# Kernel tuning notes

Measured on AMD Instinct MI355X. Metric: run time of the kernel, lower is better.

The kernel has to match this reference:

```python
import jax, jax.numpy as jnp
import numpy as np

BLOCK = 64          # block_dim
GAPS = (1, 64)      # block_dim**i for i in range(num_layers=2), input_dim=4096
N_BLOCKS = 64       # input_dim // block_dim
HID = 128           # 2 * block_dim (hidden_layers_ratio=[2])
BS = 8192
IN_DIM = 4096


def setup_inputs() -> dict:
    key = jax.random.key(0)
    kx, kw1, kw2 = jax.random.split(key, 3)
    x = jax.random.normal(kx, (BS, IN_DIM), dtype=jnp.float32)
    # one BlockResMLP per factorized layer: BlockLinear(64, 64, 128) -> ELU -> BlockLinear(64, 128, 64)
    w1 = jax.random.normal(kw1, (len(GAPS), N_BLOCKS, BLOCK, HID), dtype=jnp.float32) / np.sqrt(BLOCK)
    b1 = jnp.zeros((len(GAPS), N_BLOCKS, 1, HID), dtype=jnp.float32)
    w2 = jax.random.normal(kw2, (len(GAPS), N_BLOCKS, HID, BLOCK), dtype=jnp.float32) / np.sqrt(HID)
    b2 = jnp.zeros((len(GAPS), N_BLOCKS, 1, BLOCK), dtype=jnp.float32)
    return {"x": x, "w1": w1, "b1": b1, "w2": w2, "b2": b2}


def _facto(y, w1, b1, w2, b2):
    # BlockResMLP.forward: view(bs, n_blocks, BLOCK).transpose(0,1) -> batched block GEMMs -> residual
    bs = y.shape[0]
    z = y.reshape(bs, -1, BLOCK).transpose(1, 0, 2)              # (n_blocks, bs, BLOCK)
    h = jnp.einsum('nbd,nde->nbe', z, w1) + b1                   # BlockLinear 1 + bias
    h = jax.nn.elu(h)                                            # ELU (alpha=1)
    h = jnp.einsum('nbe,ned->nbd', h, w2) + b2                   # BlockLinear 2 + bias
    z = h + z                                                    # residual
    return z.transpose(1, 0, 2).reshape(bs, -1)


def reference(x, w1, b1, w2, b2):
    bs = x.shape[0]
    y = x
    for i, gap in enumerate(GAPS):
        # permutation shuffle: view(-1, BLOCK, gap).transpose(2,1).contiguous().view(bs,-1)
        y = y.reshape(-1, BLOCK, gap).transpose(0, 2, 1).reshape(bs, -1)
        y = _facto(y, w1[i], b1[i], w2[i], b2[i])
        # inverse shuffle: view(-1, gap, BLOCK).transpose(2,1)
        y = y.reshape(-1, gap, BLOCK).transpose(0, 2, 1).reshape(bs, -1)
    return y
```

## Files before the change

### kernel.cpp

```cpp
#include <hip/hip_runtime.h>


typedef short short8 __attribute__((ext_vector_type(8)));
typedef short short4v __attribute__((ext_vector_type(4)));
typedef float floatx4 __attribute__((ext_vector_type(4)));
typedef unsigned int uintx4 __attribute__((ext_vector_type(4)));

#define MFMA(A, B, C) __builtin_amdgcn_mfma_f32_16x16x32_bf16((A), (B), (C), 0, 0, 0)

__device__ __forceinline__ unsigned short bf16r(float f) {
  unsigned int u = __builtin_bit_cast(unsigned int, f);
  u += 0x7FFFu + ((u >> 16) & 1u);
  return (unsigned short)(u >> 16);
}
__device__ __forceinline__ float bf16f(unsigned short h) {
  unsigned int u = ((unsigned int)h) << 16;
  return __builtin_bit_cast(float, u);
}
__device__ __forceinline__ unsigned int pk2(float lo, float hi) {
  return (unsigned int)bf16r(lo) | ((unsigned int)bf16r(hi) << 16);
}
__device__ __forceinline__ float eluf(float v) {
  return v > 0.f ? v : (__expf(v) - 1.f);
}
__device__ __forceinline__ uint4 gather44(const short* A, const short* B, int s) {
  uint4 o;
  o.x = (unsigned int)(unsigned short)A[0 * s] |
        ((unsigned int)(unsigned short)A[1 * s] << 16);
  o.y = (unsigned int)(unsigned short)A[2 * s] |
        ((unsigned int)(unsigned short)A[3 * s] << 16);
  o.z = (unsigned int)(unsigned short)B[0 * s] |
        ((unsigned int)(unsigned short)B[1 * s] << 16);
  o.w = (unsigned int)(unsigned short)B[2 * s] |
        ((unsigned int)(unsigned short)B[3 * s] << 16);
  return o;
}

__global__ __launch_bounds__(256) void k0_prep(const float* __restrict__ w1,
                                               const float* __restrict__ w2,
                                               short* __restrict__ w1t,
                                               short* __restrict__ w2t) {
  __shared__ __align__(16) short T[128 * 72];
  const int t  = threadIdx.x;
  const int ln = blockIdx.x >> 1;
  const bool pm = (ln >= 64);
  if ((blockIdx.x & 1) == 0) {
    const float* src = w1 + (size_t)ln * 8192 + t * 32;
    const int d = t >> 2, e0 = (t & 3) * 32;
#pragma unroll
    for (int u = 0; u < 32; u += 2) {
      *(unsigned int*)&T[d * 136 + e0 + u] = pk2(src[u], src[u + 1]);
    }
    __syncthreads();
    const int e = t >> 1, d0 = (t & 1) * 32;
    short* dst = w1t + (size_t)ln * 8192 + e * 64 + d0;
#pragma unroll
    for (int k = 0; k < 4; ++k) {
      const int ta = d0 + (pm ? 4 * k : 8 * k);
      const int tb = d0 + (pm ? 16 + 4 * k : 8 * k + 4);
      *(uint4*)(dst + k * 8) = gather44(&T[ta * 136 + e], &T[tb * 136 + e], 136);
    }
  } else {
    const float* src = w2 + (size_t)ln * 8192 + t * 32;
    const int e = t >> 1, d0 = (t & 1) * 32;
#pragma unroll
    for (int u = 0; u < 32; u += 2) {
      *(unsigned int*)&T[e * 72 + d0 + u] = pk2(src[u], src[u + 1]);
    }
    __syncthreads();
    const int dp = t >> 2, e0 = (t & 3) * 32;
    short* dst = w2t + (size_t)ln * 8192 + dp * 128 + e0;
#pragma unroll
    for (int k = 0; k < 4; ++k) {
      const int ta = e0 + (pm ? 4 * k : 8 * k);
      const int tb = e0 + (pm ? 16 + 4 * k : 8 * k + 4);
      *(uint4*)(dst + k * 8) = gather44(&T[ta * 72 + dp], &T[tb * 72 + dp], 72);
    }
  }
}

__global__ __launch_bounds__(256) void k1_layer0(
    const float* __restrict__ x,
    const short* __restrict__ w1t, const short* __restrict__ w2t,
    const float* __restrict__ b1,  const float* __restrict__ b2,
    short* __restrict__ y1) {
  __shared__ __align__(16) short hst[4][2][16][72];
  const int tid  = threadIdx.x;
  const int lane = tid & 63;
  const int wv   = tid >> 6;
  const int il   = lane & 15;
  const int q    = lane >> 4;
  const int npair   = blockIdx.x & 31;
  const int rowtile = blockIdx.x >> 5;
  const int n  = npair * 2 + (wv & 1);
  const int r0 = rowtile * 64 + (wv >> 1) * 32;

  const short* w1n = w1t + (size_t)n * 8192;
  const short* w2n = w2t + (size_t)n * 8192;
  const float* b1n = b1 + n * 128;
  const float* b2n = b2 + n * 64;

  short8 a[2][2];
#pragma unroll
  for (int Mt = 0; Mt < 2; ++Mt) {
#pragma unroll
    for (int ks = 0; ks < 2; ++ks) {
      const float* xp = x + (size_t)(r0 + Mt * 16 + il) * 4096 + n * 64 + ks * 32 + q * 8;
      floatx4 f0 = *(const floatx4*)xp;
      floatx4 f1 = *(const floatx4*)(xp + 4);
      short8 t;
#pragma unroll
      for (int u = 0; u < 4; ++u) { t[u] = (short)bf16r(f0[u]); t[4 + u] = (short)bf16r(f1[u]); }
      a[ks][Mt] = t;
    }
  }

  floatx4 acc2[2][4] = {};
  for (int hh = 0; hh < 2; ++hh) {
    floatx4 acc1[2][4] = {};
#pragma unroll
    for (int ks = 0; ks < 2; ++ks) {
#pragma unroll
      for (int nt = 0; nt < 4; ++nt) {
        short8 b = *(const short8*)(w1n + (hh * 64 + nt * 16 + il) * 64 + ks * 32 + q * 8);
        acc1[0][nt] = MFMA(a[ks][0], b, acc1[0][nt]);
        acc1[1][nt] = MFMA(a[ks][1], b, acc1[1][nt]);
      }
    }
#pragma unroll
    for (int nt = 0; nt < 4; ++nt) {
      float bias = b1n[hh * 64 + nt * 16 + il];
#pragma unroll
      for (int Mt = 0; Mt < 2; ++Mt)
#pragma unroll
        for (int rg = 0; rg < 4; ++rg) {
          float v = acc1[Mt][nt][rg] + bias;
          hst[wv][Mt][q * 4 + rg][nt * 16 + il] = (short)bf16r(eluf(v));
        }
    }
    asm volatile("s_waitcnt lgkmcnt(0)" ::: "memory");
#pragma unroll
    for (int ks2 = 0; ks2 < 2; ++ks2) {
      short8 a2[2];
      a2[0] = *(const short8*)&hst[wv][0][il][ks2 * 32 + q * 8];
      a2[1] = *(const short8*)&hst[wv][1][il][ks2 * 32 + q * 8];
#pragma unroll
      for (int nt2 = 0; nt2 < 4; ++nt2) {
        short8 b = *(const short8*)(w2n + (nt2 * 16 + il) * 128 + hh * 64 + ks2 * 32 + q * 8);
        acc2[0][nt2] = MFMA(a2[0], b, acc2[0][nt2]);
        acc2[1][nt2] = MFMA(a2[1], b, acc2[1][nt2]);
      }
    }
    asm volatile("s_waitcnt lgkmcnt(0)" ::: "memory");
  }
#pragma unroll
  for (int Mt = 0; Mt < 2; ++Mt) {
    const int R0 = r0 + Mt * 16 + q * 4;
    const size_t nbase = ((size_t)((r0 + Mt * 16) >> 4) * 64 + n) * 64;
#pragma unroll
    for (int nt2 = 0; nt2 < 4; ++nt2) {
      const int j = nt2 * 16 + il;
      const float bias = b2n[j];
      float v0 = acc2[Mt][nt2][0] + bias + x[(size_t)(R0 + 0) * 4096 + n * 64 + j];
      float v1 = acc2[Mt][nt2][1] + bias + x[(size_t)(R0 + 1) * 4096 + n * 64 + j];
      float v2 = acc2[Mt][nt2][2] + bias + x[(size_t)(R0 + 2) * 4096 + n * 64 + j];
      float v3 = acc2[Mt][nt2][3] + bias + x[(size_t)(R0 + 3) * 4096 + n * 64 + j];
      uint2 pk;
      pk.x = pk2(v0, v1);
      pk.y = pk2(v2, v3);
      *(uint2*)(y1 + (nbase + j) * 16 + q * 4) = pk;
    }
  }
}

#define RSTR 1156
#define ISTR 18
__global__ __launch_bounds__(256) void k2_layer1_out(
    const short* __restrict__ y1,
    const short* __restrict__ w1t, const short* __restrict__ w2t,
    const float* __restrict__ b1,  const float* __restrict__ b2,
    float* __restrict__ out) {
  __shared__ __align__(16) short yo[16 * RSTR];
  const int tid  = threadIdx.x;
  const int lane = tid & 63;
  const int wv   = tid >> 6;
  const int il   = lane & 15;
  const int q    = lane >> 4;
  const int G    = blockIdx.x & 511;
  const int m0   = (blockIdx.x >> 9) * 16;

  short8 pb;
#pragma unroll
  for (int v = 0; v < 8; ++v) pb[v] = (v < 4 && il == q * 4 + v) ? (short)0x3F80 : (short)0;
  const floatx4 zero4 = {0.f, 0.f, 0.f, 0.f};

#pragma unroll
  for (int mi = 0; mi < 4; ++mi) {
    const int ml = wv * 4 + mi;
    const int m  = m0 + ml;
    const short* w1m = w1t + (size_t)(64 + m) * 8192;
    const short* w2m = w2t + (size_t)(64 + m) * 8192;
    const float* b1m = b1 + (64 + m) * 128;
    const float* b2m = b2 + (64 + m) * 64;

    short4v za[4];
#pragma unroll
    for (int nt = 0; nt < 4; ++nt)
      za[nt] = *(const short4v*)(y1 + ((size_t)(G * 64 + nt * 16 + il) * 64 + m) * 16 + q * 4);

    floatx4 zd[4];
#pragma unroll
    for (int nt = 0; nt < 4; ++nt) {
      short8 az = {za[nt][0], za[nt][1], za[nt][2], za[nt][3], 0, 0, 0, 0};
      zd[nt] = MFMA(az, pb, zero4);
    }
    short8 at[2];
#pragma unroll
    for (int ks = 0; ks < 2; ++ks) {
      uintx4 w;
      w[0] = pk2(zd[2 * ks][0], zd[2 * ks][1]);
      w[1] = pk2(zd[2 * ks][2], zd[2 * ks][3]);
      w[2] = pk2(zd[2 * ks + 1][0], zd[2 * ks + 1][1]);
      w[3] = pk2(zd[2 * ks + 1][2], zd[2 * ks + 1][3]);
      at[ks] = __builtin_bit_cast(short8, w);
    }

    floatx4 acc2[4] = {};
    uintx4 a2w[4];
#pragma unroll
    for (int hh = 0; hh < 2; ++hh) {
      floatx4 acc1[4] = {};
#pragma unroll
      for (int ks = 0; ks < 2; ++ks)
#pragma unroll
        for (int nt = 0; nt < 4; ++nt) {
          short8 b = *(const short8*)(w1m + (hh * 64 + nt * 16 + il) * 64 + ks * 32 + q * 8);
          acc1[nt] = MFMA(at[ks], b, acc1[nt]);
        }
#pragma unroll
      for (int nt = 0; nt < 4; ++nt) {
        const float bias = b1m[hh * 64 + nt * 16 + il];
        short8 ha = {(short)bf16r(eluf(acc1[nt][0] + bias)),
                     (short)bf16r(eluf(acc1[nt][1] + bias)),
                     (short)bf16r(eluf(acc1[nt][2] + bias)),
                     (short)bf16r(eluf(acc1[nt][3] + bias)),
                     0, 0, 0, 0};
        floatx4 hd = MFMA(ha, pb, zero4);
        const int ks2 = hh * 2 + (nt >> 1);
        const int hf  = nt & 1;
        a2w[ks2][hf * 2 + 0] = pk2(hd[0], hd[1]);
        a2w[ks2][hf * 2 + 1] = pk2(hd[2], hd[3]);
      }
    }
#pragma unroll
    for (int ks2 = 0; ks2 < 4; ++ks2) {
      short8 af = __builtin_bit_cast(short8, a2w[ks2]);
#pragma unroll
      for (int nt2 = 0; nt2 < 4; ++nt2) {
        short8 b = *(const short8*)(w2m + (nt2 * 16 + il) * 128 + ks2 * 32 + q * 8);
        acc2[nt2] = MFMA(af, b, acc2[nt2]);
      }
    }
#pragma unroll
    for (int nt2 = 0; nt2 < 4; ++nt2) {
      const int i = nt2 * 16 + il;
      const float bias = b2m[i];
#pragma unroll
      for (int rg = 0; rg < 4; ++rg) {
        float val = acc2[nt2][rg] + bias + bf16f((unsigned short)za[nt2][rg]);
        yo[(q * 4 + rg) * RSTR + i * ISTR + ml] = (short)bf16r(val);
      }
    }
  }
  __syncthreads();

  const int r  = tid & 15;
  const int i0 = (tid >> 4) * 4;
  float* orow = out + (size_t)(G * 16 + r) * 4096 + m0;
#pragma unroll
  for (int k = 0; k < 4; ++k) {
    const int i = i0 + k;
    const short* yr = &yo[r * RSTR + i * ISTR];
    float f[16];
#pragma unroll
    for (int j = 0; j < 8; ++j) {
      unsigned int w = *(const unsigned int*)(yr + 2 * j);
      f[2 * j]     = bf16f((unsigned short)(w & 0xffffu));
      f[2 * j + 1] = bf16f((unsigned short)(w >> 16));
    }
    float* op = orow + i * 64;
    *(floatx4*)(op + 0)  = (floatx4){f[0],  f[1],  f[2],  f[3]};
    *(floatx4*)(op + 4)  = (floatx4){f[4],  f[5],  f[6],  f[7]};
    *(floatx4*)(op + 8)  = (floatx4){f[8],  f[9],  f[10], f[11]};
    *(floatx4*)(op + 12) = (floatx4){f[12], f[13], f[14], f[15]};
  }
}

extern "C" void kernel_launch(void* const* d_in, const int* in_sizes, int n_in,
                              void* d_out, int out_size, void* d_ws, size_t ws_size,
                              hipStream_t stream) {
  const float* x  = (const float*)d_in[0];
  const float* w1 = (const float*)d_in[1];
  const float* b1 = (const float*)d_in[2];
  const float* w2 = (const float*)d_in[3];
  const float* b2 = (const float*)d_in[4];
  float* out = (float*)d_out;

  short* w1t = (short*)d_ws;
  short* w2t = w1t + (1u << 20);
  short* y1  = w2t + (1u << 20);

  hipLaunchKernelGGL(k0_prep,       dim3(256),  dim3(256), 0, stream, w1, w2, w1t, w2t);
  hipLaunchKernelGGL(k1_layer0,     dim3(4096), dim3(256), 0, stream, x, w1t, w2t, b1, b2, y1);
  hipLaunchKernelGGL(k2_layer1_out, dim3(2048), dim3(256), 0, stream, y1, w1t, w2t, b1, b2, out);
}
```

Measured before the change: 466.7 us.

## Keep layer-0 hidden activations in registers and restructure layer-1 output blocks

Layer 0 now re-lays out the ELU hidden tile through a permutation MFMA instead of an LDS round trip, and rebuilds the residual from the already-loaded bf16 input fragments instead of re-reading fp32 x from global memory. The w2 prep always uses the permuted k-order to match the new A-fragment layout. Layer 1 moves to 1024-thread blocks where each wave owns one block index m across four row groups, with double-buffered LDS staging and a sync per group so output stores are 16-byte coalesced per row. The residual now uses bf16-rounded x, which changes numerics slightly, and the per-group barriers add synchronisation.

```diff
diff --git a/kernel.cpp b/kernel.cpp
--- a/kernel.cpp
+++ b/kernel.cpp
@@ -43,8 +43,8 @@
   __shared__ __align__(16) short T[128 * 72];
   const int t  = threadIdx.x;
   const int ln = blockIdx.x >> 1;
-  const bool pm = (ln >= 64);
   if ((blockIdx.x & 1) == 0) {
+    const bool pm = (ln >= 64);
     const float* src = w1 + (size_t)ln * 8192 + t * 32;
     const int d = t >> 2, e0 = (t & 3) * 32;
 #pragma unroll
@@ -72,8 +72,8 @@
     short* dst = w2t + (size_t)ln * 8192 + dp * 128 + e0;
 #pragma unroll
     for (int k = 0; k < 4; ++k) {
-      const int ta = e0 + (pm ? 4 * k : 8 * k);
-      const int tb = e0 + (pm ? 16 + 4 * k : 8 * k + 4);
+      const int ta = e0 + 4 * k;
+      const int tb = e0 + 16 + 4 * k;
       *(uint4*)(dst + k * 8) = gather44(&T[ta * 72 + dp], &T[tb * 72 + dp], 72);
     }
   }
@@ -84,7 +84,6 @@
     const short* __restrict__ w1t, const short* __restrict__ w2t,
     const float* __restrict__ b1,  const float* __restrict__ b2,
     short* __restrict__ y1) {
-  __shared__ __align__(16) short hst[4][2][16][72];
   const int tid  = threadIdx.x;
   const int lane = tid & 63;
   const int wv   = tid >> 6;
@@ -100,6 +99,11 @@
   const float* b1n = b1 + n * 128;
   const float* b2n = b2 + n * 64;
 
+  const floatx4 zero4 = {0.f, 0.f, 0.f, 0.f};
+  short8 pbH;
+#pragma unroll
+  for (int v = 0; v < 8; ++v) pbH[v] = (v < 4 && il == q * 4 + v) ? (short)0x3F80 : (short)0;
+
   short8 a[2][2];
 #pragma unroll
   for (int Mt = 0; Mt < 2; ++Mt) {
@@ -127,91 +131,113 @@
         acc1[1][nt] = MFMA(a[ks][1], b, acc1[1][nt]);
       }
     }
-#pragma unroll
-    for (int nt = 0; nt < 4; ++nt) {
-      float bias = b1n[hh * 64 + nt * 16 + il];
-#pragma unroll
-      for (int Mt = 0; Mt < 2; ++Mt)
-#pragma unroll
-        for (int rg = 0; rg < 4; ++rg) {
-          float v = acc1[Mt][nt][rg] + bias;
-          hst[wv][Mt][q * 4 + rg][nt * 16 + il] = (short)bf16r(eluf(v));
-        }
-    }
-    asm volatile("s_waitcnt lgkmcnt(0)" ::: "memory");
-#pragma unroll
-    for (int ks2 = 0; ks2 < 2; ++ks2) {
-      short8 a2[2];
-      a2[0] = *(const short8*)&hst[wv][0][il][ks2 * 32 + q * 8];
-      a2[1] = *(const short8*)&hst[wv][1][il][ks2 * 32 + q * 8];
+    uintx4 a2w[2][2];
+#pragma unroll
+    for (int Mt = 0; Mt < 2; ++Mt) {
+#pragma unroll
+      for (int nt = 0; nt < 4; ++nt) {
+        const float bias = b1n[hh * 64 + nt * 16 + il];
+        short8 ha = {(short)bf16r(eluf(acc1[Mt][nt][0] + bias)),
+                     (short)bf16r(eluf(acc1[Mt][nt][1] + bias)),
+                     (short)bf16r(eluf(acc1[Mt][nt][2] + bias)),
+                     (short)bf16r(eluf(acc1[Mt][nt][3] + bias)),
+                     0, 0, 0, 0};
+        floatx4 hd = MFMA(ha, pbH, zero4);
+        const int ks2l = nt >> 1;
+        const int hf   = nt & 1;
+        a2w[Mt][ks2l][hf * 2 + 0] = pk2(hd[0], hd[1]);
+        a2w[Mt][ks2l][hf * 2 + 1] = pk2(hd[2], hd[3]);
+      }
+    }
+#pragma unroll
+    for (int ks2l = 0; ks2l < 2; ++ks2l) {
+      short8 af0 = __builtin_bit_cast(short8, a2w[0][ks2l]);
+      short8 af1 = __builtin_bit_cast(short8, a2w[1][ks2l]);
 #pragma unroll
       for (int nt2 = 0; nt2 < 4; ++nt2) {
-        short8 b = *(const short8*)(w2n + (nt2 * 16 + il) * 128 + hh * 64 + ks2 * 32 + q * 8);
-        acc2[0][nt2] = MFMA(a2[0], b, acc2[0][nt2]);
-        acc2[1][nt2] = MFMA(a2[1], b, acc2[1][nt2]);
-      }
-    }
-    asm volatile("s_waitcnt lgkmcnt(0)" ::: "memory");
+        short8 b = *(const short8*)(w2n + (nt2 * 16 + il) * 128 + hh * 64 + ks2l * 32 + q * 8);
+        acc2[0][nt2] = MFMA(af0, b, acc2[0][nt2]);
+        acc2[1][nt2] = MFMA(af1, b, acc2[1][nt2]);
+      }
+    }
+  }
+
+  short8 pb0, pb1;
+#pragma unroll
+  for (int v = 0; v < 8; ++v) {
+    pb0[v] = (q * 8 + v == il)      ? (short)0x3F80 : (short)0;
+    pb1[v] = (q * 8 + v == il + 16) ? (short)0x3F80 : (short)0;
   }
 #pragma unroll
   for (int Mt = 0; Mt < 2; ++Mt) {
-    const int R0 = r0 + Mt * 16 + q * 4;
     const size_t nbase = ((size_t)((r0 + Mt * 16) >> 4) * 64 + n) * 64;
 #pragma unroll
-    for (int nt2 = 0; nt2 < 4; ++nt2) {
-      const int j = nt2 * 16 + il;
-      const float bias = b2n[j];
-      float v0 = acc2[Mt][nt2][0] + bias + x[(size_t)(R0 + 0) * 4096 + n * 64 + j];
-      float v1 = acc2[Mt][nt2][1] + bias + x[(size_t)(R0 + 1) * 4096 + n * 64 + j];
-      float v2 = acc2[Mt][nt2][2] + bias + x[(size_t)(R0 + 2) * 4096 + n * 64 + j];
-      float v3 = acc2[Mt][nt2][3] + bias + x[(size_t)(R0 + 3) * 4096 + n * 64 + j];
-      uint2 pk;
-      pk.x = pk2(v0, v1);
-      pk.y = pk2(v2, v3);
-      *(uint2*)(y1 + (nbase + j) * 16 + q * 4) = pk;
+    for (int ks = 0; ks < 2; ++ks) {
+      floatx4 xr[2];
+      xr[0] = MFMA(a[ks][Mt], pb0, zero4);
+      xr[1] = MFMA(a[ks][Mt], pb1, zero4);
+#pragma unroll
+      for (int h = 0; h < 2; ++h) {
+        const int nt2 = ks * 2 + h;
+        const int j = nt2 * 16 + il;
+        const float bias = b2n[j];
+        uint2 pk;
+        pk.x = pk2(acc2[Mt][nt2][0] + bias + xr[h][0],
+                   acc2[Mt][nt2][1] + bias + xr[h][1]);
+        pk.y = pk2(acc2[Mt][nt2][2] + bias + xr[h][2],
+                   acc2[Mt][nt2][3] + bias + xr[h][3]);
+        *(uint2*)(y1 + (nbase + j) * 16 + q * 4) = pk;
+      }
     }
   }
 }
 
 #define RSTR 1156
 #define ISTR 18
-__global__ __launch_bounds__(256) void k2_layer1_out(
+__global__ __launch_bounds__(1024) void k2_layer1_out(
     const short* __restrict__ y1,
     const short* __restrict__ w1t, const short* __restrict__ w2t,
     const float* __restrict__ b1,  const float* __restrict__ b2,
     float* __restrict__ out) {
-  __shared__ __align__(16) short yo[16 * RSTR];
+  __shared__ __align__(16) short yo[2][16 * RSTR];
   const int tid  = threadIdx.x;
   const int lane = tid & 63;
   const int wv   = tid >> 6;
   const int il   = lane & 15;
   const int q    = lane >> 4;
-  const int G    = blockIdx.x & 511;
-  const int m0   = (blockIdx.x >> 9) * 16;
+  const int rowband = blockIdx.x & 127;
+  const int m0      = (blockIdx.x >> 7) * 16;
+  const int m       = m0 + wv;
 
   short8 pb;
 #pragma unroll
   for (int v = 0; v < 8; ++v) pb[v] = (v < 4 && il == q * 4 + v) ? (short)0x3F80 : (short)0;
   const floatx4 zero4 = {0.f, 0.f, 0.f, 0.f};
 
-#pragma unroll
-  for (int mi = 0; mi < 4; ++mi) {
-    const int ml = wv * 4 + mi;
-    const int m  = m0 + ml;
-    const short* w1m = w1t + (size_t)(64 + m) * 8192;
-    const short* w2m = w2t + (size_t)(64 + m) * 8192;
-    const float* b1m = b1 + (64 + m) * 128;
-    const float* b2m = b2 + (64 + m) * 64;
-
-    short4v za[4];
+  const short* w1m = w1t + (size_t)(64 + m) * 8192;
+  const short* w2m = w2t + (size_t)(64 + m) * 8192;
+  const float* b1m = b1 + (64 + m) * 128;
+  const float* b2m = b2 + (64 + m) * 64;
+
+  short4v za[4][4];
+#pragma unroll
+  for (int g = 0; g < 4; ++g) {
+    const int G = rowband * 4 + g;
 #pragma unroll
     for (int nt = 0; nt < 4; ++nt)
-      za[nt] = *(const short4v*)(y1 + ((size_t)(G * 64 + nt * 16 + il) * 64 + m) * 16 + q * 4);
-
+      za[g][nt] = *(const short4v*)(y1 + ((size_t)(G * 64 + nt * 16 + il) * 64 + m) * 16 + q * 4);
+  }
+
+  const int fmq = tid & 3;
+  const int fiw = (tid >> 2) & 63;
+  const int frr = tid >> 8;
+
+#pragma unroll
+  for (int g = 0; g < 4; ++g) {
     floatx4 zd[4];
 #pragma unroll
     for (int nt = 0; nt < 4; ++nt) {
-      short8 az = {za[nt][0], za[nt][1], za[nt][2], za[nt][3], 0, 0, 0, 0};
+      short8 az = {za[g][nt][0], za[g][nt][1], za[g][nt][2], za[g][nt][3], 0, 0, 0, 0};
       zd[nt] = MFMA(az, pb, zero4);
     }
     short8 at[2];
@@ -261,38 +287,33 @@
         acc2[nt2] = MFMA(af, b, acc2[nt2]);
       }
     }
+    short* yob = &yo[g & 1][0];
 #pragma unroll
     for (int nt2 = 0; nt2 < 4; ++nt2) {
       const int i = nt2 * 16 + il;
       const float bias = b2m[i];
 #pragma unroll
       for (int rg = 0; rg < 4; ++rg) {
-        float val = acc2[nt2][rg] + bias + bf16f((unsigned short)za[nt2][rg]);
-        yo[(q * 4 + rg) * RSTR + i * ISTR + ml] = (short)bf16r(val);
-      }
-    }
-  }
-  __syncthreads();
-
-  const int r  = tid & 15;
-  const int i0 = (tid >> 4) * 4;
-  float* orow = out + (size_t)(G * 16 + r) * 4096 + m0;
-#pragma unroll
-  for (int k = 0; k < 4; ++k) {
-    const int i = i0 + k;
-    const short* yr = &yo[r * RSTR + i * ISTR];
-    float f[16];
-#pragma unroll
-    for (int j = 0; j < 8; ++j) {
-      unsigned int w = *(const unsigned int*)(yr + 2 * j);
-      f[2 * j]     = bf16f((unsigned short)(w & 0xffffu));
-      f[2 * j + 1] = bf16f((unsigned short)(w >> 16));
-    }
-    float* op = orow + i * 64;
-    *(floatx4*)(op + 0)  = (floatx4){f[0],  f[1],  f[2],  f[3]};
-    *(floatx4*)(op + 4)  = (floatx4){f[4],  f[5],  f[6],  f[7]};
-    *(floatx4*)(op + 8)  = (floatx4){f[8],  f[9],  f[10], f[11]};
-    *(floatx4*)(op + 12) = (floatx4){f[12], f[13], f[14], f[15]};
+        float val = acc2[nt2][rg] + bias + bf16f((unsigned short)za[g][nt2][rg]);
+        yob[(q * 4 + rg) * RSTR + i * ISTR + wv] = (short)bf16r(val);
+      }
+    }
+    __syncthreads();
+    {
+      const int G = rowband * 4 + g;
+#pragma unroll
+      for (int p = 0; p < 4; ++p) {
+        const int r = p * 4 + frr;
+        const short* yr = &yo[g & 1][r * RSTR + fiw * ISTR + fmq * 4];
+        unsigned int w0 = *(const unsigned int*)(yr);
+        unsigned int w1_ = *(const unsigned int*)(yr + 2);
+        floatx4 vv = {bf16f((unsigned short)(w0 & 0xffffu)),
+                      bf16f((unsigned short)(w0 >> 16)),
+                      bf16f((unsigned short)(w1_ & 0xffffu)),
+                      bf16f((unsigned short)(w1_ >> 16))};
+        *(floatx4*)(out + (size_t)(G * 16 + r) * 4096 + fiw * 64 + m0 + fmq * 4) = vv;
+      }
+    }
   }
 }
 
@@ -310,7 +331,7 @@
   short* w2t = w1t + (1u << 20);
   short* y1  = w2t + (1u << 20);
 
-  hipLaunchKernelGGL(k0_prep,       dim3(256),  dim3(256), 0, stream, w1, w2, w1t, w2t);
-  hipLaunchKernelGGL(k1_layer0,     dim3(4096), dim3(256), 0, stream, x, w1t, w2t, b1, b2, y1);
-  hipLaunchKernelGGL(k2_layer1_out, dim3(2048), dim3(256), 0, stream, y1, w1t, w2t, b1, b2, out);
-}
+  hipLaunchKernelGGL(k0_prep,       dim3(256),  dim3(256),  0, stream, w1, w2, w1t, w2t);
+  hipLaunchKernelGGL(k1_layer0,     dim3(4096), dim3(256),  0, stream, x, w1t, w2t, b1, b2, y1);
+  hipLaunchKernelGGL(k2_layer1_out, dim3(512),  dim3(1024), 0, stream, y1, w1t, w2t, b1, b2, out);
+}
```

After: 481.7 us. 1.03x slower.
